# Optimization experiments

Measured on AMD Instinct MI355X. Metric: run time of the kernel, lower is better.

The kernel has to match this reference:

```python
import jax, jax.numpy as jnp
import numpy as np

NHEAD = 8
NPTS = 4
LN_EPS = 1e-5


def pos_embed(H, W, nf):
    # create_pos_embedding with normalize=True, temperature=10000, scale=2*pi
    scale = 2.0 * np.pi
    eps = 1e-6
    y_e = jnp.arange(1, H + 1, dtype=jnp.float32)
    y_e = y_e / (y_e[-1] + eps) * scale
    x_e = jnp.arange(1, W + 1, dtype=jnp.float32)
    x_e = x_e / (x_e[-1] + eps) * scale
    i = jnp.arange(nf, dtype=jnp.float32)
    dim_t = 10000.0 ** (2.0 * jnp.floor(i / 2.0) / nf)
    def enc(e):
        p = e[:, None] / dim_t  # [len, nf]
        return jnp.stack([jnp.sin(p[:, 0::2]), jnp.cos(p[:, 1::2])], axis=-1).reshape(e.shape[0], -1)
    py = enc(y_e)  # [H, nf]
    px = enc(x_e)  # [W, nf]
    pos = jnp.concatenate([
        jnp.broadcast_to(py[:, None, :], (H, W, nf)),
        jnp.broadcast_to(px[None, :, :], (H, W, nf)),
    ], axis=-1)  # [H, W, 2*nf], channel order (pos_y, pos_x) as in torch cat
    return pos.reshape(H * W, 2 * nf)


def layernorm(x, s, b):
    m = x.mean(-1, keepdims=True)
    v = x.var(-1, keepdims=True)
    return (x - m) * jax.lax.rsqrt(v + LN_EPS) * s + b


def bilinear_sample(value, loc, H, W):
    # value [B, HW, Hd, dh]; loc [B, Q, Hd, P, 2] normalized to [0,1] (x, y)
    # Matches F.grid_sample(align_corners=False, padding_mode='zeros') with grid = 2*loc - 1
    B, HW, Hd, dh = value.shape
    Q = loc.shape[1]
    v = value.transpose(0, 2, 1, 3)  # [B, Hd, HW, dh]
    x = loc[..., 0] * W - 0.5
    y = loc[..., 1] * H - 0.5
    x0 = jnp.floor(x)
    y0 = jnp.floor(y)
    wx1 = x - x0
    wy1 = y - y0
    x0i = x0.astype(jnp.int32)
    y0i = y0.astype(jnp.int32)
    def t(a):  # [B, Q, Hd, P] -> [B, Hd, Q*P]
        return a.transpose(0, 2, 1, 3).reshape(B, Hd, -1)
    def gather(xi, yi):
        valid = ((xi >= 0) & (xi < W) & (yi >= 0) & (yi < H)).astype(v.dtype)
        idx = jnp.clip(yi, 0, H - 1) * W + jnp.clip(xi, 0, W - 1)
        g = jnp.take_along_axis(v, t(idx)[..., None], axis=2)  # [B, Hd, Q*P, dh]
        return g * t(valid)[..., None]
    g00 = gather(x0i, y0i)
    g10 = gather(x0i + 1, y0i)
    g01 = gather(x0i, y0i + 1)
    g11 = gather(x0i + 1, y0i + 1)
    out = (g00 * t((1 - wx1) * (1 - wy1))[..., None]
           + g10 * t(wx1 * (1 - wy1))[..., None]
           + g01 * t((1 - wx1) * wy1)[..., None]
           + g11 * t(wx1 * wy1)[..., None])
    return out.reshape(B, Hd, Q, NPTS, dh)


def _forward(x, merge_w, merge_b, off_w, off_b, aw_w, aw_b, val_w, val_b, out_w, out_b,
             n1_s, n1_b, l1_w, l1_b, l2_w, l2_b, n2_s, n2_b, outc_w, outc_b):
    B, N, C, H, W = x.shape
    D = merge_w.shape[0]
    dh = D // NHEAD
    Q = H * W
    # merge: 1x1 conv + relu
    src = jax.nn.relu(jnp.einsum('bchw,dc->bhwd', x.reshape(B, N * C, H, W), merge_w) + merge_b)
    src = src.reshape(B, Q, D)
    pos = pos_embed(H, W, D // 2)[None].astype(x.dtype)  # [1, Q, D]
    # reference points (valid_ratios = 1): centers of cells, normalized
    ys = (jnp.arange(H, dtype=x.dtype) + 0.5) / H
    xs = (jnp.arange(W, dtype=x.dtype) + 0.5) / W
    gx, gy = jnp.meshgrid(xs, ys, indexing='xy')  # each [H, W]
    ref = jnp.stack([gx, gy], axis=-1).reshape(1, Q, 2)
    norm = jnp.array([W, H], dtype=x.dtype)  # offset normalizer (W, H) for (x, y)
    n_layers = off_w.shape[0]
    for l in range(n_layers):
        q = src + pos
        off = (q @ off_w[l] + off_b[l]).reshape(B, Q, NHEAD, NPTS, 2)
        aw = jax.nn.softmax((q @ aw_w[l] + aw_b[l]).reshape(B, Q, NHEAD, NPTS), axis=-1)
        val = (src @ val_w[l] + val_b[l]).reshape(B, Q, NHEAD, dh)
        loc = ref[:, :, None, None, :] + off / norm  # [B, Q, Hd, P, 2]
        samp = bilinear_sample(val, loc, H, W)  # [B, Hd, Q, P, dh]
        o = (samp * aw.transpose(0, 2, 1, 3)[..., None]).sum(3)  # [B, Hd, Q, dh]
        o = o.transpose(0, 2, 1, 3).reshape(B, Q, D) @ out_w[l] + out_b[l]
        src = layernorm(src + o, n1_s[l], n1_b[l])
        ff = jax.nn.relu(src @ l1_w[l] + l1_b[l]) @ l2_w[l] + l2_b[l]
        src = layernorm(src + ff, n2_s[l], n2_b[l])
    feat = src.reshape(B, H, W, D)
    out = jax.nn.relu(jnp.einsum('bhwc,dc->bhwd', feat, outc_w) + outc_b)
    return out.transpose(0, 3, 1, 2)  # [B, D, H, W]


def setup_inputs() -> dict:
    key = jax.random.key(0)
    B, N, Cb, H, W = 1, 4, 128, 120, 360
    D, Dff, L = 128, 512, 3
    ks = jax.random.split(key, 12)
    def rn(k, shape, s=0.02):
        return jax.random.normal(k, shape, dtype=jnp.float32) * s
    return {
        'x': jax.random.normal(ks[0], (B, N, Cb, H, W), dtype=jnp.float32),
        'merge_w': rn(ks[1], (D, N * Cb)),
        'merge_b': jnp.zeros((D,), jnp.float32),
        'off_w': rn(ks[2], (L, D, NHEAD * NPTS * 2)),
        'off_b': rn(ks[3], (L, NHEAD * NPTS * 2), 0.5),
        'aw_w': rn(ks[4], (L, D, NHEAD * NPTS)),
        'aw_b': jnp.zeros((L, NHEAD * NPTS), jnp.float32),
        'val_w': rn(ks[5], (L, D, D)),
        'val_b': jnp.zeros((L, D), jnp.float32),
        'out_w': rn(ks[6], (L, D, D)),
        'out_b': jnp.zeros((L, D), jnp.float32),
        'n1_s': jnp.ones((L, D), jnp.float32),
        'n1_b': jnp.zeros((L, D), jnp.float32),
        'l1_w': rn(ks[7], (L, D, Dff)),
        'l1_b': jnp.zeros((L, Dff), jnp.float32),
        'l2_w': rn(ks[8], (L, Dff, D)),
        'l2_b': jnp.zeros((L, D), jnp.float32),
        'n2_s': jnp.ones((L, D), jnp.float32),
        'n2_b': jnp.zeros((L, D), jnp.float32),
        'outc_w': rn(ks[9], (D, D)),
        'outc_b': jnp.zeros((D,), jnp.float32),
    }


def reference(x, merge_w, merge_b, off_w, off_b, aw_w, aw_b, val_w, val_b, out_w, out_b,
              n1_s, n1_b, l1_w, l1_b, l2_w, l2_b, n2_s, n2_b, outc_w, outc_b):
    return _forward(x, merge_w, merge_b, off_w, off_b, aw_w, aw_b, val_w, val_b, out_w, out_b,
                    n1_s, n1_b, l1_w, l1_b, l2_w, l2_b, n2_s, n2_b, outc_w, outc_b)
```

## Files before the change

kernel.cpp:

```cpp
#include <hip/hip_runtime.h>
#include <hip/hip_bf16.h>
#include <math.h>

#define Q_TOT 43200
#define H_ 120
#define W_ 360

typedef unsigned short ushort_t;
typedef float f32x4 __attribute__((ext_vector_type(4)));
typedef unsigned short u16x2 __attribute__((ext_vector_type(2)));
typedef unsigned short u16x4 __attribute__((ext_vector_type(4)));
typedef unsigned short u16x8 __attribute__((ext_vector_type(8)));
using short8 = __attribute__((ext_vector_type(8))) short;

static __device__ __forceinline__ float b2f(unsigned short u){
  return __uint_as_float(((unsigned)u) << 16);
}
static __device__ __forceinline__ unsigned short f2b(float f){
  unsigned u = __float_as_uint(f);
  unsigned r = (u + 0x7fffu + ((u >> 16) & 1u)) >> 16;
  return (unsigned short)r;
}

#define SWZ(row, byte) ((byte) ^ (((row) & 7) << 4))
#define SWZ3(row, byte) ((byte) ^ ((((row) ^ ((row) >> 3)) & 7) << 4))

#define CVT_TOT 615072
__global__ __launch_bounds__(256) void cvt_kernel(
    const float* p0, const float* p1, const float* p2, const float* p3,
    const float* p4, const float* p5, const float* p6, const float* p7,
    const float* p8, const float* p9, const float* p10, const float* p11,
    const float* p12, const float* p13, const float* p14, const float* p15,
    const float* p16, const float* p17, const float* p18, const float* p19,
    ushort_t* __restrict__ dst){
  const float* ps[20] = {p0,p1,p2,p3,p4,p5,p6,p7,p8,p9,p10,p11,p12,p13,p14,p15,p16,p17,p18,p19};
  const int offs[20] = {0,65536,65664,90240,90432,102720,102816,151968,152352,201504,
                        201888,202272,202656,399264,400800,597408,597792,598176,598560,614944};
  int gid = blockIdx.x*256 + threadIdx.x;
  if (gid >= CVT_TOT) return;
  int s = 0;
  #pragma unroll
  for (int i=1;i<20;i++) s += (gid >= offs[i]) ? 1 : 0;
  dst[gid] = f2b(ps[s][gid - offs[s]]);
}

#define CVTT_TOT 528384
__global__ __launch_bounds__(256) void cvtT_kernel(
    const float* __restrict__ vw, const float* __restrict__ ow,
    const float* __restrict__ w1, const float* __restrict__ w2,
    const float* __restrict__ offw, const float* __restrict__ aww,
    ushort_t* __restrict__ dst){
  int gid = blockIdx.x*256 + threadIdx.x;
  if (gid >= CVTT_TOT) return;
  if (gid >= 491520){
    int e = gid - 491520;
    int l = e / 12288, rem = e - l*12288;
    int n = rem >> 7, k = rem & 127;
    float v = (n < 64) ? offw[((size_t)l*128 + k)*64 + n]
                       : aww [((size_t)l*128 + k)*32 + (n-64)];
    dst[gid] = f2b(v);
    return;
  }
  const float* s; int K, N, off;
  if (gid < 49152)      { s = vw; K = 128; N = 128; off = 0; }
  else if (gid < 98304) { s = ow; K = 128; N = 128; off = 49152; }
  else if (gid < 294912){ s = w1; K = 128; N = 512; off = 98304; }
  else                  { s = w2; K = 512; N = 128; off = 294912; }
  int e = gid - off;
  int per = K*N;
  int l = e / per, rem = e - l*per;
  int n = rem / K, k = rem - n*K;
  dst[gid] = f2b(s[(size_t)l*per + (size_t)k*N + n]);
}

__global__ __launch_bounds__(256) void postab_kernel(float* __restrict__ tab){
  int gid = blockIdx.x*256 + threadIdx.x;
  if (gid >= 480*64) return;
  int row = gid >> 6, k = gid & 63;
  int m = k >> 1;
  float t = powf(10000.0f, (float)m * (1.0f/32.0f));
  float e;
  if (row < 120) e = (float)(row+1)   * (6.283185307179586f/((float)H_+1e-6f));
  else           e = (float)(row-119) * (6.283185307179586f/((float)W_+1e-6f));
  float p = e / t;
  tab[gid] = (k & 1) ? cosf(p) : sinf(p);
}

__global__ __launch_bounds__(256, 4) void merge_mfma(const float* __restrict__ x,
    const ushort_t* __restrict__ mw,
    const ushort_t* __restrict__ mb,
    ushort_t* __restrict__ srcbf){
  __shared__ ushort_t xt[2][32*128];
  const int tid = threadIdx.x;
  const int wave = tid >> 6, lane = tid & 63;
  const int lr = lane & 15, kg = lane >> 4;
  const int q0 = blockIdx.x * 32;
  const int qq4 = (tid & 7) * 4;
  const int c4  = (tid >> 3) * 4;
  const int qh = wave & 1, dq = wave >> 1;
  const int qrow = qh*16 + lr;

  f32x4 v[4];
  #pragma unroll
  for (int cc=0;cc<4;cc++)
    v[cc] = *(const f32x4*)(x + (size_t)(c4 + cc)*Q_TOT + q0 + qq4);
  #pragma unroll
  for (int qq=0;qq<4;qq++){
    int row = qq4 + qq;
    u16x4 pk;
    #pragma unroll
    for (int cc=0;cc<4;cc++) pk[cc] = f2b(v[cc][qq]);
    *(u16x4*)((char*)xt[0] + SWZ3(row, row*256 + c4*2)) = pk;
  }
  __syncthreads();

  f32x4 acc[4];
  #pragma unroll
  for (int i=0;i<4;i++) acc[i] = (f32x4){0.f,0.f,0.f,0.f};

  for (int ch = 0; ch < 4; ch++){
    f32x4 v2[4];
    if (ch < 3){
      #pragma unroll
      for (int cc=0;cc<4;cc++)
        v2[cc] = *(const f32x4*)(x + (size_t)((ch+1)*128 + c4 + cc)*Q_TOT + q0 + qq4);
    }
    const ushort_t* xb = xt[ch & 1];
    short8 xfc[4];
    #pragma unroll
    for (int ks=0; ks<4; ks++)
      xfc[ks] = *(const short8*)((const char*)xb + SWZ3(qrow, qrow*256 + (ks*32 + kg*8)*2));
    short8 wfr[2][4];
    #pragma unroll
    for (int ks=0; ks<4; ks++)
      wfr[0][ks] = *(const short8*)(mw + (size_t)(dq*64 + lr)*512 + ch*128 + ks*32 + kg*8);
    #pragma unroll
    for (int dtl=0; dtl<4; dtl++){
      if (dtl < 3){
        const int nr = (dq*4 + dtl+1)*16 + lr;
        #pragma unroll
        for (int ks=0; ks<4; ks++)
          wfr[(dtl+1)&1][ks] = *(const short8*)(mw + (size_t)nr*512 + ch*128 + ks*32 + kg*8);
      }
      #pragma unroll
      for (int ks=0; ks<4; ks++)
        acc[dtl] = __builtin_amdgcn_mfma_f32_16x16x32_bf16(xfc[ks], wfr[dtl&1][ks], acc[dtl], 0, 0, 0);
    }
    if (ch < 3){
      ushort_t* xn = xt[(ch+1) & 1];
      #pragma unroll
      for (int qq=0;qq<4;qq++){
        int row = qq4 + qq;
        u16x4 pk;
        #pragma unroll
        for (int cc=0;cc<4;cc++) pk[cc] = f2b(v2[cc][qq]);
        *(u16x4*)((char*)xn + SWZ3(row, row*256 + c4*2)) = pk;
      }
      __syncthreads();
    }
  }
  #pragma unroll
  for (int dtl=0; dtl<4; dtl++){
    int d = (dq*4 + dtl)*16 + lr;
    float bb = b2f(mb[d]);
    #pragma unroll
    for (int r=0; r<4; r++){
      int q = q0 + qh*16 + kg*4 + r;
      float vv = acc[dtl][r] + bb;
      srcbf[(size_t)q*128 + d] = f2b(vv > 0.f ? vv : 0.f);
    }
  }
}

__global__ __launch_bounds__(256, 3) void qv_mfma(const ushort_t* __restrict__ srcbf,
    const float* __restrict__ py, const float* __restrict__ px,
    const ushort_t* __restrict__ owt,
    const ushort_t* __restrict__ ob, const ushort_t* __restrict__ awb,
    const ushort_t* __restrict__ vwt,
    const ushort_t* __restrict__ vb,
    float* __restrict__ loc, float* __restrict__ awg,
    ushort_t* __restrict__ valbf){
  __shared__ ushort_t a_lds[64*128];
  __shared__ ushort_t qlds[64*128];
  const int tid = threadIdx.x;
  const int wave = tid >> 6, lane = tid & 63;
  const int lr = lane & 15, kg = lane >> 4;
  const int q0 = blockIdx.x * 64;
  #pragma unroll
  for (int i=0;i<4;i++){
    int idx = i*256 + tid;
    int row = idx >> 4, ch = idx & 15;
    int q = q0 + row, qy = q / W_, qx = q - qy*W_;
    u16x8 s = *(const u16x8*)(srcbf + (size_t)q*128 + ch*8);
    int c0 = ch*8;
    const float* tp = (c0 < 64) ? (py + qy*64 + c0) : (px + qx*64 + (c0-64));
    f32x4 t0 = *(const f32x4*)tp, t1 = *(const f32x4*)(tp+4);
    u16x8 pq;
    #pragma unroll
    for (int j=0;j<4;j++){
      pq[j]   = f2b(b2f(s[j])   + t0[j]);
      pq[4+j] = f2b(b2f(s[4+j]) + t1[j]);
    }
    int byte = row*256 + c0*2;
    *(u16x8*)((char*)a_lds + SWZ(row, byte)) = s;
    *(u16x8*)((char*)qlds + SWZ(row, byte)) = pq;
  }
  __syncthreads();
  const int qrow = wave*16 + lr;
  short8 xf[4], xq[4];
  #pragma unroll
  for (int ks=0; ks<4; ks++){
    xf[ks] = *(const short8*)((const char*)a_lds + SWZ(qrow, qrow*256 + (ks*32+kg*8)*2));
    xq[ks] = *(const short8*)((const char*)qlds + SWZ(qrow, qrow*256 + (ks*32+kg*8)*2));
  }
  f32x4 va[8];
  #pragma unroll
  for (int dt=0; dt<8; dt++) va[dt] = (f32x4){0.f,0.f,0.f,0.f};
  short8 yf[2][4];
  #pragma unroll
  for (int ks=0; ks<4; ks++)
    yf[0][ks] = *(const short8*)(vwt + (size_t)lr*128 + ks*32 + kg*8);
  #pragma unroll
  for (int dt=0; dt<8; dt++){
    if (dt < 7){
      const int nr = (dt+1)*16 + lr;
      #pragma unroll
      for (int ks=0; ks<4; ks++)
        yf[(dt+1)&1][ks] = *(const short8*)(vwt + (size_t)nr*128 + ks*32 + kg*8);
    }
    #pragma unroll
    for (int ks=0; ks<4; ks++)
      va[dt] = __builtin_amdgcn_mfma_f32_16x16x32_bf16(xf[ks], yf[dt&1][ks], va[dt], 0, 0, 0);
  }
  f32x4 qa[6];
  #pragma unroll
  for (int nt=0; nt<6; nt++) qa[nt] = (f32x4){0.f,0.f,0.f,0.f};
  short8 of[2][4];
  #pragma unroll
  for (int ks=0; ks<4; ks++)
    of[0][ks] = *(const short8*)(owt + (size_t)lr*128 + ks*32 + kg*8);
  #pragma unroll
  for (int nt=0; nt<6; nt++){
    if (nt < 5){
      const int nr = (nt+1)*16 + lr;
      #pragma unroll
      for (int ks=0; ks<4; ks++)
        of[(nt+1)&1][ks] = *(const short8*)(owt + (size_t)nr*128 + ks*32 + kg*8);
    }
    #pragma unroll
    for (int ks=0; ks<4; ks++)
      qa[nt] = __builtin_amdgcn_mfma_f32_16x16x32_bf16(xq[ks], of[nt&1][ks], qa[nt], 0, 0, 0);
  }
  #pragma unroll
  for (int dt=0; dt<8; dt++){
    float bb = b2f(vb[dt*16 + lr]);
    #pragma unroll
    for (int r=0; r<4; r++){
      int q = q0 + wave*16 + kg*4 + r;
      valbf[(size_t)q*128 + dt*16 + lr] = f2b(va[dt][r] + bb);
    }
  }
  #pragma unroll
  for (int r=0; r<4; r++){
    int q = q0 + wave*16 + kg*4 + r;
    int qy = q / W_, qx = q - qy*W_;
    float qxf = (float)qx, qyf = (float)qy;
    #pragma unroll
    for (int dt=0; dt<4; dt++){
      int n = dt*16 + lr;
      float v = qa[dt][r] + b2f(ob[n]);
      loc[(size_t)q*64 + n] = ((n & 1) ? qyf : qxf) + v;
    }
    #pragma unroll
    for (int d4=0; d4<2; d4++){
      int idx = d4*16 + lr;
      float v = qa[4+d4][r] + b2f(awb[idx]);
      float mx = fmaxf(v, __shfl_xor(v, 1, 64));
      mx = fmaxf(mx, __shfl_xor(mx, 2, 64));
      float e = expf(v - mx);
      float s = e + __shfl_xor(e, 1, 64);
      s = s + __shfl_xor(s, 2, 64);
      awg[(size_t)q*32 + idx] = e / s;
    }
  }
}

__global__ __launch_bounds__(256) void sample_kernel(const ushort_t* __restrict__ val,
    const float* __restrict__ loc, const float* __restrict__ awg,
    ushort_t* __restrict__ obf){
  __shared__ float sl[4][64];
  __shared__ float sa[4][32];
  const int tid = threadIdx.x;
  const int q0 = blockIdx.x * 4;
  sl[0][tid & 255] = loc[(size_t)q0*64 + tid];
  if (tid < 128) sa[0][tid] = awg[(size_t)q0*32 + tid];
  __syncthreads();
  const int ql = tid >> 6, cp = (tid & 63) * 2;
  const int h = cp >> 4;
  float a0 = 0.f, a1 = 0.f;
  #pragma unroll
  for (int p=0;p<4;p++){
    float x = sl[ql][h*8 + p*2];
    float y = sl[ql][h*8 + p*2 + 1];
    float wgt = sa[ql][h*4 + p];
    float x0f = floorf(x), y0f = floorf(y);
    float wx = x - x0f, wy = y - y0f;
    int ix = (int)x0f, iy = (int)y0f;
    int x0c = min(max(ix, 0), W_-1),   x1c = min(max(ix+1, 0), W_-1);
    int y0c = min(max(iy, 0), H_-1),   y1c = min(max(iy+1, 0), H_-1);
    float vx0 = (ix   >= 0 && ix   < W_) ? 1.f : 0.f;
    float vx1 = (ix+1 >= 0 && ix+1 < W_) ? 1.f : 0.f;
    float vy0 = (iy   >= 0 && iy   < H_) ? 1.f : 0.f;
    float vy1 = (iy+1 >= 0 && iy+1 < H_) ? 1.f : 0.f;
    float w00 = (1.f-wx)*(1.f-wy)*vx0*vy0 * wgt;
    float w10 = wx*(1.f-wy)*vx1*vy0 * wgt;
    float w01 = (1.f-wx)*wy*vx0*vy1 * wgt;
    float w11 = wx*wy*vx1*vy1 * wgt;
    unsigned g00 = *(const unsigned*)(val + (size_t)(y0c*W_ + x0c)*128 + cp);
    unsigned g10 = *(const unsigned*)(val + (size_t)(y0c*W_ + x1c)*128 + cp);
    unsigned g01 = *(const unsigned*)(val + (size_t)(y1c*W_ + x0c)*128 + cp);
    unsigned g11 = *(const unsigned*)(val + (size_t)(y1c*W_ + x1c)*128 + cp);
    a0 += w00*b2f((ushort_t)g00) + w10*b2f((ushort_t)g10)
        + w01*b2f((ushort_t)g01) + w11*b2f((ushort_t)g11);
    a1 += w00*b2f((ushort_t)(g00>>16)) + w10*b2f((ushort_t)(g10>>16))
        + w01*b2f((ushort_t)(g01>>16)) + w11*b2f((ushort_t)(g11>>16));
  }
  unsigned pk = (unsigned)f2b(a0) | ((unsigned)f2b(a1) << 16);
  *(unsigned*)&obf[(size_t)(q0+ql)*128 + cp] = pk;
}

__global__ __launch_bounds__(256, 3) void outln_mfma(const ushort_t* __restrict__ obf,
    const ushort_t* __restrict__ wt,
    const ushort_t* __restrict__ bias,
    const ushort_t* __restrict__ gs, const ushort_t* __restrict__ gb,
    ushort_t* srcbf){
  __shared__ char smem[16896];
  ushort_t* a_lds = (ushort_t*)smem;
  float* scr = (float*)smem;
  const int tid = threadIdx.x;
  const int wave = tid >> 6, lane = tid & 63;
  const int lr = lane & 15, kg = lane >> 4;
  const int q0 = blockIdx.x * 32;
  const int qh = wave >> 1, nh = wave & 1;
  #pragma unroll
  for (int i=0;i<2;i++){
    int idx = i*256 + tid;
    int row = idx >> 4, ch = idx & 15;
    u16x8 s = *(const u16x8*)(obf + (size_t)(q0+row)*128 + ch*8);
    *(u16x8*)((char*)a_lds + SWZ(row, row*256 + ch*16)) = s;
  }
  __syncthreads();
  const int qrow = qh*16 + lr;
  short8 xf[4];
  #pragma unroll
  for (int ks=0; ks<4; ks++)
    xf[ks] = *(const short8*)((const char*)a_lds + SWZ(qrow, qrow*256 + (ks*32+kg*8)*2));
  __syncthreads();
  f32x4 acc[4];
  #pragma unroll
  for (int i=0;i<4;i++) acc[i] = (f32x4){0.f,0.f,0.f,0.f};
  short8 yf[2][4];
  #pragma unroll
  for (int ks=0; ks<4; ks++)
    yf[0][ks] = *(const short8*)(wt + (size_t)((nh*4)*16+lr)*128 + ks*32 + kg*8);
  #pragma unroll
  for (int dtl=0; dtl<4; dtl++){
    if (dtl < 3){
      const int nr = (nh*4+dtl+1)*16 + lr;
      #pragma unroll
      for (int ks=0; ks<4; ks++)
        yf[(dtl+1)&1][ks] = *(const short8*)(wt + (size_t)nr*128 + ks*32 + kg*8);
    }
    #pragma unroll
    for (int ks=0; ks<4; ks++)
      acc[dtl] = __builtin_amdgcn_mfma_f32_16x16x32_bf16(xf[ks], yf[dtl&1][ks], acc[dtl], 0, 0, 0);
  }
  #pragma unroll
  for (int dtl=0; dtl<4; dtl++)
    #pragma unroll
    for (int r=0; r<4; r++)
      scr[(qh*16 + kg*4 + r)*132 + nh*64 + dtl*16 + lr] = acc[dtl][r];
  __syncthreads();
  {
    const int c = lane*2;
    float bi0 = b2f(bias[c]), bi1 = b2f(bias[c+1]);
    float g0  = b2f(gs[c]),   g1  = b2f(gs[c+1]);
    float be0 = b2f(gb[c]),   be1 = b2f(gb[c+1]);
    #pragma unroll
    for (int i=0; i<8; i++){
      int ql = wave*8 + i;
      unsigned rr = *(const unsigned*)(srcbf + (size_t)(q0+ql)*128 + c);
      float v0 = scr[ql*132 + c]     + bi0 + b2f((ushort_t)rr);
      float v1 = scr[ql*132 + c + 1] + bi1 + b2f((ushort_t)(rr >> 16));
      float s1 = v0 + v1, s2 = v0*v0 + v1*v1;
      #pragma unroll
      for (int m=1; m<64; m<<=1){ s1 += __shfl_xor(s1, m, 64); s2 += __shfl_xor(s2, m, 64); }
      float mean = s1*(1.f/128.f);
      float var  = s2*(1.f/128.f) - mean*mean;
      float inv  = rsqrtf(var + 1e-5f);
      float o0 = (v0-mean)*inv*g0 + be0;
      float o1 = (v1-mean)*inv*g1 + be1;
      unsigned pk = (unsigned)f2b(o0) | ((unsigned)f2b(o1) << 16);
      *(unsigned*)(srcbf + (size_t)(q0+ql)*128 + c) = pk;
    }
  }
}

__global__ __launch_bounds__(512, 2) void ffn_mfma(
    const ushort_t* __restrict__ w1t,
    const ushort_t* __restrict__ b1,
    const ushort_t* __restrict__ w2t,
    const ushort_t* __restrict__ b2,
    const ushort_t* __restrict__ gs, const ushort_t* __restrict__ gb,
    ushort_t* srcbf){
  __shared__ char smem[24576];
  ushort_t* a_lds = (ushort_t*)smem;
  ushort_t* h_lds = (ushort_t*)(smem + 8192);
  float* scr = (float*)smem;
  const int tid = threadIdx.x;
  const int wave = tid >> 6, lane = tid & 63;
  const int lr = lane & 15, kg = lane >> 4;
  const int q0 = blockIdx.x * 32;
  {
    int row = tid >> 4, ch = tid & 15;
    u16x8 s = *(const u16x8*)(srcbf + (size_t)(q0+row)*128 + ch*8);
    *(u16x8*)((char*)a_lds + SWZ(row, row*256 + ch*16)) = s;
  }
  const int drow = wave*16 + lr;
  f32x4 accd[2];
  accd[0] = (f32x4){0.f,0.f,0.f,0.f};
  accd[1] = (f32x4){0.f,0.f,0.f,0.f};
  __syncthreads();
  for (int half=0; half<2; half++){
    short8 wf[2][4];
    #pragma unroll
    for (int nt=0; nt<2; nt++){
      const int nrow = (half*16 + wave*2 + nt)*16 + lr;
      #pragma unroll
      for (int ks=0; ks<4; ks++)
        wf[nt][ks] = *(const short8*)(w1t + (size_t)nrow*128 + ks*32 + kg*8);
    }
    short8 yg[8];
    #pragma unroll
    for (int ks=0; ks<8; ks++)
      yg[ks] = *(const short8*)(w2t + (size_t)drow*512 + half*256 + ks*32 + kg*8);
    #pragma unroll
    for (int nt=0; nt<2; nt++){
      const int ngt = half*16 + wave*2 + nt;
      u16x4 bb = *(const u16x4*)(b1 + ngt*16 + kg*4);
      float bf[4];
      #pragma unroll
      for (int j=0;j<4;j++) bf[j] = b2f(bb[j]);
      #pragma unroll
      for (int qt=0; qt<2; qt++){
        f32x4 acc = (f32x4){0.f,0.f,0.f,0.f};
        const int q = qt*16 + lr;
        #pragma unroll
        for (int ks=0; ks<4; ks++){
          short8 yf = *(const short8*)((const char*)a_lds + SWZ(q, q*256 + (ks*32 + kg*8)*2));
          acc = __builtin_amdgcn_mfma_f32_16x16x32_bf16(wf[nt][ks], yf, acc, 0, 0, 0);
        }
        const int nl = (ngt & 15)*16 + kg*4;
        u16x4 hp;
        #pragma unroll
        for (int r=0;r<4;r++){ float v = acc[r] + bf[r]; hp[r] = f2b(v > 0.f ? v : 0.f); }
        *(u16x4*)((char*)h_lds + SWZ(q, q*512 + nl*2)) = hp;
      }
    }
    __syncthreads();
    #pragma unroll
    for (int qt=0; qt<2; qt++){
      const int qrow = qt*16 + lr;
      short8 xh[8];
      #pragma unroll
      for (int ks=0; ks<8; ks++)
        xh[ks] = *(const short8*)((const char*)h_lds + SWZ(qrow, qrow*512 + (ks*32 + kg*8)*2));
      #pragma unroll
      for (int ks=0; ks<8; ks++)
        accd[qt] = __builtin_amdgcn_mfma_f32_16x16x32_bf16(xh[ks], yg[ks], accd[qt], 0, 0, 0);
    }
    __syncthreads();
  }
  #pragma unroll
  for (int qt=0; qt<2; qt++)
    #pragma unroll
    for (int r=0; r<4; r++)
      scr[(qt*16 + kg*4 + r)*132 + wave*16 + lr] = accd[qt][r];
  __syncthreads();
  {
    const int c = lane*2;
    float bi0 = b2f(b2[c]), bi1 = b2f(b2[c+1]);
    float g0  = b2f(gs[c]), g1  = b2f(gs[c+1]);
    float be0 = b2f(gb[c]), be1 = b2f(gb[c+1]);
    #pragma unroll
    for (int i=0; i<4; i++){
      int ql = wave*4 + i;
      unsigned rr = *(const unsigned*)(srcbf + (size_t)(q0+ql)*128 + c);
      float v0 = scr[ql*132 + c]     + bi0 + b2f((ushort_t)rr);
      float v1 = scr[ql*132 + c + 1] + bi1 + b2f((ushort_t)(rr >> 16));
      float s1 = v0 + v1, s2 = v0*v0 + v1*v1;
      #pragma unroll
      for (int m=1; m<64; m<<=1){ s1 += __shfl_xor(s1, m, 64); s2 += __shfl_xor(s2, m, 64); }
      float mean = s1*(1.f/128.f);
      float var  = s2*(1.f/128.f) - mean*mean;
      float inv  = rsqrtf(var + 1e-5f);
      float o0 = (v0-mean)*inv*g0 + be0;
      float o1 = (v1-mean)*inv*g1 + be1;
      unsigned pk = (unsigned)f2b(o0) | ((unsigned)f2b(o1) << 16);
      *(unsigned*)(srcbf + (size_t)(q0+ql)*128 + c) = pk;
    }
  }
}

__global__ __launch_bounds__(256, 3) void outc_mfma(const ushort_t* __restrict__ srcbf,
    const ushort_t* __restrict__ wt,
    const ushort_t* __restrict__ bias,
    float* __restrict__ outp){
  __shared__ ushort_t a_lds[64*128];
  const int tid = threadIdx.x;
  const int wave = tid >> 6, lane = tid & 63;
  const int lr = lane & 15, kg = lane >> 4;
  const int q0 = blockIdx.x * 64;
  #pragma unroll
  for (int i=0;i<4;i++){
    int idx = i*256 + tid;
    int row = idx >> 4, ch = idx & 15;
    u16x8 s = *(const u16x8*)(srcbf + (size_t)(q0+row)*128 + ch*8);
    *(u16x8*)((char*)a_lds + SWZ(row, row*256 + ch*16)) = s;
  }
  __syncthreads();
  const int qrow = wave*16 + lr;
  short8 xf[4];
  #pragma unroll
  for (int ks=0; ks<4; ks++)
    xf[ks] = *(const short8*)((const char*)a_lds + SWZ(qrow, qrow*256 + (ks*32+kg*8)*2));
  f32x4 acc[8];
  #pragma unroll
  for (int dt=0; dt<8; dt++) acc[dt] = (f32x4){0.f,0.f,0.f,0.f};
  short8 yf[2][4];
  #pragma unroll
  for (int ks=0; ks<4; ks++)
    yf[0][ks] = *(const short8*)(wt + (size_t)lr*128 + ks*32 + kg*8);
  #pragma unroll
  for (int dt=0; dt<8; dt++){
    if (dt < 7){
      const int nr = (dt+1)*16 + lr;
      #pragma unroll
      for (int ks=0; ks<4; ks++)
        yf[(dt+1)&1][ks] = *(const short8*)(wt + (size_t)nr*128 + ks*32 + kg*8);
    }
    #pragma unroll
    for (int ks=0; ks<4; ks++)
      acc[dt] = __builtin_amdgcn_mfma_f32_16x16x32_bf16(xf[ks], yf[dt&1][ks], acc[dt], 0, 0, 0);
  }
  #pragma unroll
  for (int dt=0; dt<8; dt++){
    float bb = b2f(bias[dt*16 + lr]);
    #pragma unroll
    for (int r=0; r<4; r++){
      int q = q0 + wave*16 + kg*4 + r;
      float v = acc[dt][r] + bb;
      v = v > 0.f ? v : 0.f;
      outp[(size_t)(dt*16 + lr)*Q_TOT + q] = v;
    }
  }
}

extern "C" void kernel_launch(void* const* d_in, const int* in_sizes, int n_in,
                              void* d_out, int out_size, void* d_ws, size_t ws_size,
                              hipStream_t stream){
  const float* x = (const float*)d_in[0];

  ushort_t* srcbf = (ushort_t*)d_ws;
  ushort_t* obf   = srcbf + (size_t)Q_TOT*128;
  ushort_t* valbf = obf   + (size_t)Q_TOT*128;
  float* loc = (float*)(valbf + (size_t)Q_TOT*128);
  float* aw  = loc + (size_t)Q_TOT*64;
  ushort_t* wbf   = (ushort_t*)(aw + (size_t)Q_TOT*32);
  ushort_t* tbase = wbf + 615072;
  float* postab = (float*)(tbase + 528384);
  float* pytab = postab;
  float* pxtab = postab + 120*64;

  const ushort_t* mw     = wbf + 0;
  const ushort_t* mb     = wbf + 65536;
  const ushort_t* off_b  = wbf + 90240;
  const ushort_t* aw_b   = wbf + 102720;
  const ushort_t* val_b  = wbf + 151968;
  const ushort_t* out_b  = wbf + 201504;
  const ushort_t* n1_s   = wbf + 201888;
  const ushort_t* n1_b   = wbf + 202272;
  const ushort_t* l1_b   = wbf + 399264;
  const ushort_t* l2_b   = wbf + 597408;
  const ushort_t* n2_s   = wbf + 597792;
  const ushort_t* n2_b   = wbf + 598176;
  const ushort_t* outc_w = wbf + 598560;
  const ushort_t* outc_b = wbf + 614944;
  const ushort_t* val_wt = tbase + 0;
  const ushort_t* out_wt = tbase + 49152;
  const ushort_t* l1_wt  = tbase + 98304;
  const ushort_t* l2_wt  = tbase + 294912;
  const ushort_t* oaw_t  = tbase + 491520;

  cvt_kernel<<<(CVT_TOT+255)/256, 256, 0, stream>>>(
      (const float*)d_in[1],  (const float*)d_in[2],  (const float*)d_in[3],
      (const float*)d_in[4],  (const float*)d_in[5],  (const float*)d_in[6],
      (const float*)d_in[7],  (const float*)d_in[8],  (const float*)d_in[9],
      (const float*)d_in[10], (const float*)d_in[11], (const float*)d_in[12],
      (const float*)d_in[13], (const float*)d_in[14], (const float*)d_in[15],
      (const float*)d_in[16], (const float*)d_in[17], (const float*)d_in[18],
      (const float*)d_in[19], (const float*)d_in[20], wbf);
  cvtT_kernel<<<CVTT_TOT/256, 256, 0, stream>>>(
      (const float*)d_in[7], (const float*)d_in[9],
      (const float*)d_in[13], (const float*)d_in[15],
      (const float*)d_in[3], (const float*)d_in[5], tbase);
  postab_kernel<<<120, 256, 0, stream>>>(postab);

  merge_mfma<<<Q_TOT/32, 256, 0, stream>>>(x, mw, mb, srcbf);
  for (int l = 0; l < 3; l++){
    qv_mfma<<<Q_TOT/64, 256, 0, stream>>>(srcbf, pytab, pxtab,
        oaw_t + (size_t)l*96*128, off_b + (size_t)l*64, aw_b + (size_t)l*32,
        val_wt + (size_t)l*128*128, val_b + (size_t)l*128,
        loc, aw, valbf);
    sample_kernel<<<Q_TOT/4, 256, 0, stream>>>(valbf, loc, aw, obf);
    outln_mfma<<<Q_TOT/32, 256, 0, stream>>>(obf,
        out_wt + (size_t)l*128*128, out_b + (size_t)l*128,
        n1_s + (size_t)l*128, n1_b + (size_t)l*128, srcbf);
    ffn_mfma<<<Q_TOT/32, 512, 0, stream>>>(
        l1_wt + (size_t)l*512*128, l1_b + (size_t)l*512,
        l2_wt + (size_t)l*128*512, l2_b + (size_t)l*128,
        n2_s + (size_t)l*128, n2_b + (size_t)l*128, srcbf);
  }
  outc_mfma<<<Q_TOT/64, 256, 0, stream>>>(srcbf, outc_w, outc_b, (float*)d_out);
}
```

Before: 447.8 us.

## Process 64 queries per block in outln and ffn, fuse LayerNorm in registers

Both the output-projection+LayerNorm kernel and the FFN kernel now handle 64 queries per block instead of 32, halving the grid and reusing each weight fragment loaded from global memory across twice as many rows. In outln, each wave computes all 128 output columns for its 16 rows, so the LDS scratch round-trip and extra barriers are dropped and LayerNorm is done from accumulators with a 16-lane shuffle reduction. The costs are higher register pressure (8 accumulators), scattered 2-byte residual loads and stores in outln, and doubled LDS in ffn with a raised occupancy hint that may not be reachable.

After: 384.7 us. 14.1% less time.

```diff
diff --git a/kernel.cpp b/kernel.cpp
--- a/kernel.cpp
+++ b/kernel.cpp
@@ -334,102 +334,95 @@
     const ushort_t* __restrict__ bias,
     const ushort_t* __restrict__ gs, const ushort_t* __restrict__ gb,
     ushort_t* srcbf){
-  __shared__ char smem[16896];
-  ushort_t* a_lds = (ushort_t*)smem;
-  float* scr = (float*)smem;
+  __shared__ ushort_t a_lds[64*128];
   const int tid = threadIdx.x;
   const int wave = tid >> 6, lane = tid & 63;
   const int lr = lane & 15, kg = lane >> 4;
-  const int q0 = blockIdx.x * 32;
-  const int qh = wave >> 1, nh = wave & 1;
-  #pragma unroll
-  for (int i=0;i<2;i++){
+  const int q0 = blockIdx.x * 64;
+  #pragma unroll
+  for (int i=0;i<4;i++){
     int idx = i*256 + tid;
     int row = idx >> 4, ch = idx & 15;
     u16x8 s = *(const u16x8*)(obf + (size_t)(q0+row)*128 + ch*8);
     *(u16x8*)((char*)a_lds + SWZ(row, row*256 + ch*16)) = s;
   }
   __syncthreads();
-  const int qrow = qh*16 + lr;
+  const int qrow = wave*16 + lr;
   short8 xf[4];
   #pragma unroll
   for (int ks=0; ks<4; ks++)
     xf[ks] = *(const short8*)((const char*)a_lds + SWZ(qrow, qrow*256 + (ks*32+kg*8)*2));
-  __syncthreads();
-  f32x4 acc[4];
-  #pragma unroll
-  for (int i=0;i<4;i++) acc[i] = (f32x4){0.f,0.f,0.f,0.f};
+  f32x4 acc[8];
+  #pragma unroll
+  for (int dt=0; dt<8; dt++) acc[dt] = (f32x4){0.f,0.f,0.f,0.f};
   short8 yf[2][4];
   #pragma unroll
   for (int ks=0; ks<4; ks++)
-    yf[0][ks] = *(const short8*)(wt + (size_t)((nh*4)*16+lr)*128 + ks*32 + kg*8);
-  #pragma unroll
-  for (int dtl=0; dtl<4; dtl++){
-    if (dtl < 3){
-      const int nr = (nh*4+dtl+1)*16 + lr;
+    yf[0][ks] = *(const short8*)(wt + (size_t)lr*128 + ks*32 + kg*8);
+  #pragma unroll
+  for (int dt=0; dt<8; dt++){
+    if (dt < 7){
+      const int nr = (dt+1)*16 + lr;
       #pragma unroll
       for (int ks=0; ks<4; ks++)
-        yf[(dtl+1)&1][ks] = *(const short8*)(wt + (size_t)nr*128 + ks*32 + kg*8);
+        yf[(dt+1)&1][ks] = *(const short8*)(wt + (size_t)nr*128 + ks*32 + kg*8);
     }
     #pragma unroll
     for (int ks=0; ks<4; ks++)
-      acc[dtl] = __builtin_amdgcn_mfma_f32_16x16x32_bf16(xf[ks], yf[dtl&1][ks], acc[dtl], 0, 0, 0);
-  }
-  #pragma unroll
-  for (int dtl=0; dtl<4; dtl++)
-    #pragma unroll
-    for (int r=0; r<4; r++)
-      scr[(qh*16 + kg*4 + r)*132 + nh*64 + dtl*16 + lr] = acc[dtl][r];
-  __syncthreads();
-  {
-    const int c = lane*2;
-    float bi0 = b2f(bias[c]), bi1 = b2f(bias[c+1]);
-    float g0  = b2f(gs[c]),   g1  = b2f(gs[c+1]);
-    float be0 = b2f(gb[c]),   be1 = b2f(gb[c+1]);
-    #pragma unroll
-    for (int i=0; i<8; i++){
-      int ql = wave*8 + i;
-      unsigned rr = *(const unsigned*)(srcbf + (size_t)(q0+ql)*128 + c);
-      float v0 = scr[ql*132 + c]     + bi0 + b2f((ushort_t)rr);
-      float v1 = scr[ql*132 + c + 1] + bi1 + b2f((ushort_t)(rr >> 16));
-      float s1 = v0 + v1, s2 = v0*v0 + v1*v1;
-      #pragma unroll
-      for (int m=1; m<64; m<<=1){ s1 += __shfl_xor(s1, m, 64); s2 += __shfl_xor(s2, m, 64); }
-      float mean = s1*(1.f/128.f);
-      float var  = s2*(1.f/128.f) - mean*mean;
-      float inv  = rsqrtf(var + 1e-5f);
-      float o0 = (v0-mean)*inv*g0 + be0;
-      float o1 = (v1-mean)*inv*g1 + be1;
-      unsigned pk = (unsigned)f2b(o0) | ((unsigned)f2b(o1) << 16);
-      *(unsigned*)(srcbf + (size_t)(q0+ql)*128 + c) = pk;
-    }
-  }
-}
-
-__global__ __launch_bounds__(512, 2) void ffn_mfma(
+      acc[dt] = __builtin_amdgcn_mfma_f32_16x16x32_bf16(xf[ks], yf[dt&1][ks], acc[dt], 0, 0, 0);
+  }
+  float g4[8], be4[8], bi4[8];
+  #pragma unroll
+  for (int dt=0; dt<8; dt++){
+    g4[dt] = b2f(gs[dt*16+lr]); be4[dt] = b2f(gb[dt*16+lr]); bi4[dt] = b2f(bias[dt*16+lr]);
+  }
+  #pragma unroll
+  for (int r=0; r<4; r++){
+    const int q = q0 + wave*16 + kg*4 + r;
+    float vals[8];
+    float s1 = 0.f, s2 = 0.f;
+    #pragma unroll
+    for (int dt=0; dt<8; dt++){
+      float v = acc[dt][r] + bi4[dt] + b2f(srcbf[(size_t)q*128 + dt*16 + lr]);
+      vals[dt] = v; s1 += v; s2 += v*v;
+    }
+    #pragma unroll
+    for (int m=1; m<16; m<<=1){ s1 += __shfl_xor(s1, m, 64); s2 += __shfl_xor(s2, m, 64); }
+    float mean = s1*(1.f/128.f);
+    float var  = s2*(1.f/128.f) - mean*mean;
+    float inv  = rsqrtf(var + 1e-5f);
+    #pragma unroll
+    for (int dt=0; dt<8; dt++)
+      srcbf[(size_t)q*128 + dt*16 + lr] = f2b((vals[dt]-mean)*inv*g4[dt] + be4[dt]);
+  }
+}
+
+__global__ __launch_bounds__(512, 4) void ffn_mfma(
     const ushort_t* __restrict__ w1t,
     const ushort_t* __restrict__ b1,
     const ushort_t* __restrict__ w2t,
     const ushort_t* __restrict__ b2,
     const ushort_t* __restrict__ gs, const ushort_t* __restrict__ gb,
     ushort_t* srcbf){
-  __shared__ char smem[24576];
+  __shared__ char smem[49152];
   ushort_t* a_lds = (ushort_t*)smem;
-  ushort_t* h_lds = (ushort_t*)(smem + 8192);
+  ushort_t* h_lds = (ushort_t*)(smem + 16384);
   float* scr = (float*)smem;
   const int tid = threadIdx.x;
   const int wave = tid >> 6, lane = tid & 63;
   const int lr = lane & 15, kg = lane >> 4;
-  const int q0 = blockIdx.x * 32;
-  {
-    int row = tid >> 4, ch = tid & 15;
+  const int q0 = blockIdx.x * 64;
+  #pragma unroll
+  for (int i=0;i<2;i++){
+    int idx = i*512 + tid;
+    int row = idx >> 4, ch = idx & 15;
     u16x8 s = *(const u16x8*)(srcbf + (size_t)(q0+row)*128 + ch*8);
     *(u16x8*)((char*)a_lds + SWZ(row, row*256 + ch*16)) = s;
   }
   const int drow = wave*16 + lr;
-  f32x4 accd[2];
-  accd[0] = (f32x4){0.f,0.f,0.f,0.f};
-  accd[1] = (f32x4){0.f,0.f,0.f,0.f};
+  f32x4 accd[4];
+  #pragma unroll
+  for (int qt=0; qt<4; qt++) accd[qt] = (f32x4){0.f,0.f,0.f,0.f};
   __syncthreads();
   for (int half=0; half<2; half++){
     short8 wf[2][4];
@@ -452,7 +445,7 @@
       #pragma unroll
       for (int j=0;j<4;j++) bf[j] = b2f(bb[j]);
       #pragma unroll
-      for (int qt=0; qt<2; qt++){
+      for (int qt=0; qt<4; qt++){
         f32x4 acc = (f32x4){0.f,0.f,0.f,0.f};
         const int q = qt*16 + lr;
         #pragma unroll
@@ -469,7 +462,7 @@
     }
     __syncthreads();
     #pragma unroll
-    for (int qt=0; qt<2; qt++){
+    for (int qt=0; qt<4; qt++){
       const int qrow = qt*16 + lr;
       short8 xh[8];
       #pragma unroll
@@ -482,19 +475,19 @@
     __syncthreads();
   }
   #pragma unroll
-  for (int qt=0; qt<2; qt++)
+  for (int qt=0; qt<4; qt++)
     #pragma unroll
     for (int r=0; r<4; r++)
       scr[(qt*16 + kg*4 + r)*132 + wave*16 + lr] = accd[qt][r];
   __syncthreads();
   {
     const int c = lane*2;
-    float bi0 = b2f(b2[c]), bi1 = b2f(b2[c+1]);
-    float g0  = b2f(gs[c]), g1  = b2f(gs[c+1]);
-    float be0 = b2f(gb[c]), be1 = b2f(gb[c+1]);
-    #pragma unroll
-    for (int i=0; i<4; i++){
-      int ql = wave*4 + i;
+    float bi0 = b2f(b2[c]),  bi1 = b2f(b2[c+1]);
+    float g0  = b2f(gs[c]),  g1  = b2f(gs[c+1]);
+    float be0 = b2f(gb[c]),  be1 = b2f(gb[c+1]);
+    #pragma unroll
+    for (int i=0; i<8; i++){
+      const int ql = wave*8 + i;
       unsigned rr = *(const unsigned*)(srcbf + (size_t)(q0+ql)*128 + c);
       float v0 = scr[ql*132 + c]     + bi0 + b2f((ushort_t)rr);
       float v1 = scr[ql*132 + c + 1] + bi1 + b2f((ushort_t)(rr >> 16));
@@ -623,10 +616,10 @@
         val_wt + (size_t)l*128*128, val_b + (size_t)l*128,
         loc, aw, valbf);
     sample_kernel<<<Q_TOT/4, 256, 0, stream>>>(valbf, loc, aw, obf);
-    outln_mfma<<<Q_TOT/32, 256, 0, stream>>>(obf,
+    outln_mfma<<<Q_TOT/64, 256, 0, stream>>>(obf,
         out_wt + (size_t)l*128*128, out_b + (size_t)l*128,
         n1_s + (size_t)l*128, n1_b + (size_t)l*128, srcbf);
-    ffn_mfma<<<Q_TOT/32, 512, 0, stream>>>(
+    ffn_mfma<<<Q_TOT/64, 512, 0, stream>>>(
         l1_wt + (size_t)l*512*128, l1_b + (size_t)l*512,
         l2_wt + (size_t)l*128*512, l2_b + (size_t)l*128,
         n2_s + (size_t)l*128, n2_b + (size_t)l*128, srcbf);
```
